# Performance work log

Hardware: AMD Instinct MI355X
Metric: run time of the kernel (lower is better)

The kernel has to match this reference:

```python
import jax, jax.numpy as jnp
import numpy as np

BATCH_SIZE_PER_IM = 512
FG_FRACTION = 0.25
FG_THRESH = 0.5
BG_THRESH_HI = 0.5
BG_THRESH_LO = 0.0
MAX_FG = int(FG_FRACTION * BATCH_SIZE_PER_IM)  # 128


def _rand_boxes(key, shape):
    a = jax.random.uniform(key, shape + (4,), dtype=jnp.float32)
    ymin = jnp.minimum(a[..., 0], a[..., 2])
    ymax = jnp.maximum(a[..., 0], a[..., 2]) + 1e-3
    xmin = jnp.minimum(a[..., 1], a[..., 3])
    xmax = jnp.maximum(a[..., 1], a[..., 3]) + 1e-3
    return jnp.stack([ymin, xmin, ymax, xmax], axis=-1)


def setup_inputs() -> dict:
    key = jax.random.key(0)
    k1, k2, k3, k4 = jax.random.split(key, 4)
    B, N, G = 32, 8192, 128
    boxes = _rand_boxes(k1, (B, N))
    gt_boxes = _rand_boxes(k2, (B, G))
    gt_labels = jax.random.randint(k3, (B, G), 0, 91, dtype=jnp.int32)
    noise = jax.random.uniform(k4, (B, N + G), dtype=jnp.float32)
    return {"boxes": boxes, "gt_boxes": gt_boxes, "gt_labels": gt_labels, "noise": noise}


def _bbox_overlap(boxes, gt_boxes):
    # boxes: [B, M, 4], gt_boxes: [B, G, 4], layout (ymin, xmin, ymax, xmax)
    b_ymin, b_xmin, b_ymax, b_xmax = [boxes[..., i:i + 1] for i in range(4)]  # [B,M,1]
    g_ymin, g_xmin, g_ymax, g_xmax = [gt_boxes[..., i][:, None, :] for i in range(4)]  # [B,1,G]
    i_ymin = jnp.maximum(b_ymin, g_ymin)
    i_xmin = jnp.maximum(b_xmin, g_xmin)
    i_ymax = jnp.minimum(b_ymax, g_ymax)
    i_xmax = jnp.minimum(b_xmax, g_xmax)
    i_area = jnp.maximum(i_ymax - i_ymin, 0.0) * jnp.maximum(i_xmax - i_xmin, 0.0)  # [B,M,G]
    b_area = (b_ymax - b_ymin) * (b_xmax - b_xmin)           # [B,M,1]
    g_area = (g_ymax - g_ymin) * (g_xmax - g_xmin)           # [B,1,G]
    iou = i_area / (b_area + g_area - i_area)
    # padded gt boxes (filled with -1) get IoU = -1
    padding = jnp.logical_and(i_ymin < 0, i_xmin < 0)
    return jnp.where(padding, -1.0, iou)


def reference(boxes, gt_boxes, gt_labels, noise):
    boxes = jax.lax.stop_gradient(boxes)
    all_boxes = jnp.concatenate([boxes, gt_boxes], axis=1)        # [B, M=N+G, 4]
    iou = _bbox_overlap(all_boxes, gt_boxes)                      # [B, M, G]
    max_ov = jnp.max(iou, axis=2)                                 # [B, M]
    p2l = jnp.argmax(iou, axis=2).astype(jnp.int32)               # [B, M]
    box_t = jnp.take_along_axis(gt_boxes, p2l[..., None], axis=1)  # [B, M, 4]
    cls_t = jnp.take_along_axis(gt_labels, p2l, axis=1)           # [B, M]
    pos = max_ov > FG_THRESH
    neg = jnp.logical_and(max_ov >= BG_THRESH_LO, max_ov < BG_THRESH_HI)
    cls_t = jnp.where(neg, 0, cls_t)
    box_t = jnp.where(neg[..., None], 0.0, box_t)
    p2l = jnp.where(neg, 0, p2l)
    # --- balanced fg/bg subsampling (random scores provided in `noise`) ---
    pos_score = jnp.where(pos, noise, -1.0)
    kth = jax.lax.top_k(pos_score, MAX_FG)[0][:, -1:]             # [B,1] threshold
    sel_pos = jnp.logical_and(pos, pos_score >= kth)              # at most MAX_FG fg
    # selected fg get priority band 2+, bg band [0,1), rest -1
    combined = jnp.where(sel_pos, 2.0 + noise, jnp.where(neg, noise, -1.0))
    _, idx = jax.lax.top_k(combined, BATCH_SIZE_PER_IM)           # [B, K]
    rois = jnp.take_along_axis(all_boxes, idx[..., None], axis=1)      # [B, K, 4]
    sample_box_t = jnp.take_along_axis(box_t, idx[..., None], axis=1)  # [B, K, 4]
    sample_cls_t = jnp.take_along_axis(cls_t, idx, axis=1)             # [B, K]
    sample_p2l = jnp.take_along_axis(p2l, idx, axis=1)                 # [B, K]
    return sample_box_t, sample_cls_t, rois, sample_p2l
```

## Files before the change

### kernel.cpp

```cpp
#include <hip/hip_runtime.h>
#include <stdint.h>

#define BATCH 32
#define NBOX 8192
#define NGT 128
#define M (NBOX + NGT)
#define K_OUT 512
#define MAX_FG 128
#define C_CAP 256
#define S_CAP 256
#define U_CAP 1024

__device__ __forceinline__ unsigned int bkt1024(float ns) {
    unsigned int u = (unsigned int)(ns * 16777216.0f) >> 14;
    return u > 1023u ? 1023u : u;
}

__global__ __launch_bounds__(256) void iou_kernel(
    const float* __restrict__ boxes,
    const float* __restrict__ gt_boxes,
    unsigned short* __restrict__ packed)
{
    const int BPB = (M + 255) / 256;
    const int b = blockIdx.x / BPB;
    const int m = (blockIdx.x % BPB) * 256 + threadIdx.x;

    __shared__ float4 sgt[NGT];
    __shared__ float  sgarea[NGT];
    if (threadIdx.x < NGT) {
        float4 g = ((const float4*)gt_boxes)[b * NGT + threadIdx.x];
        sgt[threadIdx.x] = g;
        sgarea[threadIdx.x] = __fmul_rn(__fsub_rn(g.z, g.x), __fsub_rn(g.w, g.y));
    }
    __syncthreads();
    if (m >= M) return;

    float4 bb = (m < NBOX) ? ((const float4*)boxes)[b * NBOX + m]
                           : ((const float4*)gt_boxes)[b * NGT + (m - NBOX)];
    float b_area = __fmul_rn(__fsub_rn(bb.z, bb.x), __fsub_rn(bb.w, bb.y));

    float best = -1e30f;
    int bidx = 0;
    #pragma unroll 4
    for (int g = 0; g < NGT; ++g) {
        float4 gg = sgt[g];
        float iymin = fmaxf(bb.x, gg.x);
        float ixmin = fmaxf(bb.y, gg.y);
        float iymax = fminf(bb.z, gg.z);
        float ixmax = fminf(bb.w, gg.w);
        float ia  = __fmul_rn(fmaxf(__fsub_rn(iymax, iymin), 0.0f),
                              fmaxf(__fsub_rn(ixmax, ixmin), 0.0f));
        float den = __fsub_rn(__fadd_rn(b_area, sgarea[g]), ia);
        float iou = __fdiv_rn(ia, den);
        if (iou > best) { best = iou; bidx = g; }
    }
    bool pos = best > 0.5f;
    bool neg = (best >= 0.0f) && (best < 0.5f);
    packed[b * M + m] = (unsigned short)(bidx | (neg ? 256 : 0) | (pos ? 512 : 0));
}

__global__ __launch_bounds__(1024) void select_kernel(
    const float* __restrict__ boxes,
    const float* __restrict__ gt_boxes,
    const int*   __restrict__ gt_labels,
    const float* __restrict__ noise,
    const unsigned short* __restrict__ packed,
    float* __restrict__ out)
{
    const int b = blockIdx.x;
    const int tid = threadIdx.x;

    __shared__ float sh_ns[M];
    __shared__ unsigned int hist[1024];
    __shared__ unsigned int hist2[1024];
    __shared__ unsigned char posmask[M / 8];
    __shared__ unsigned char negmask[M / 8];
    __shared__ float4 sgt[NGT];
    __shared__ int slab[NGT];
    __shared__ float C[C_CAP];
    __shared__ unsigned short slist[S_CAP];
    __shared__ unsigned int ukey[U_CAP];
    __shared__ unsigned short um[U_CAP];
    __shared__ unsigned int sh_Bp, sh_needp, sh_cc, sh_n1a, sh_B, sh_cnt, sh_kth;

    float* out_bt  = out;
    float* out_cls = out + BATCH * K_OUT * 4;
    float* out_roi = out + BATCH * K_OUT * 5;
    float* out_p2l = out + BATCH * K_OUT * 9;

    hist[tid] = 0;
    hist2[tid] = 0;
    if (tid == 0) { sh_cc = 0; sh_n1a = 0; sh_B = 0; sh_cnt = 0; sh_kth = 0xBF800000u; }
    if (tid < NGT) {
        sgt[tid]  = ((const float4*)gt_boxes)[b * NGT + tid];
        slab[tid] = gt_labels[b * NGT + tid];
    }
    __syncthreads();

    {
        const uint4*  pk4 = (const uint4*)(packed + (size_t)b * M);
        const float4* ns4 = (const float4*)(noise + (size_t)b * M);
        for (int c = tid; c < M / 8; c += 1024) {
            uint4 pv = pk4[c];
            float4 n0 = ns4[2 * c], n1v = ns4[2 * c + 1];
            ((float4*)sh_ns)[2 * c] = n0;
            ((float4*)sh_ns)[2 * c + 1] = n1v;
            unsigned short e[8];
            e[0] = (unsigned short)(pv.x & 0xFFFF); e[1] = (unsigned short)(pv.x >> 16);
            e[2] = (unsigned short)(pv.y & 0xFFFF); e[3] = (unsigned short)(pv.y >> 16);
            e[4] = (unsigned short)(pv.z & 0xFFFF); e[5] = (unsigned short)(pv.z >> 16);
            e[6] = (unsigned short)(pv.w & 0xFFFF); e[7] = (unsigned short)(pv.w >> 16);
            float f[8] = {n0.x, n0.y, n0.z, n0.w, n1v.x, n1v.y, n1v.z, n1v.w};
            unsigned int pb = 0, nb = 0;
            #pragma unroll
            for (int k = 0; k < 8; ++k) {
                if (e[k] & 512) {
                    pb |= (1u << k);
                    atomicAdd(&hist2[bkt1024(f[k])], 1u);
                } else if (e[k] & 256) {
                    nb |= (1u << k);
                    atomicAdd(&hist[bkt1024(f[k])], 1u);
                }
            }
            posmask[c] = (unsigned char)pb;
            negmask[c] = (unsigned char)nb;
        }
    }
    __syncthreads();

    {
        const int wv = tid >> 6, ln = tid & 63;
        if (wv < 2) {
            unsigned int* H = wv ? hist2 : hist;
            unsigned int s[16];
            #pragma unroll
            for (int k = 0; k < 16; ++k) {
                unsigned int v = H[k * 64 + ln];
                #pragma unroll
                for (int off = 1; off < 64; off <<= 1) {
                    unsigned int o = __shfl_down(v, off, 64);
                    if (ln + off < 64) v += o;
                }
                s[k] = v;
            }
            unsigned int after = 0;
            #pragma unroll
            for (int k = 15; k >= 0; --k) {
                unsigned int tot = __shfl(s[k], 0, 64);
                H[k * 64 + ln] = s[k] + after;
                after += tot;
            }
        }
    }
    __syncthreads();
    const unsigned int nneg = hist[0];
    const unsigned int npos = hist2[0];

    if (npos >= MAX_FG) {
        {
            unsigned int S  = hist2[tid];
            unsigned int Sn = (tid < 1023) ? hist2[tid + 1] : 0;
            if (S >= MAX_FG && Sn < MAX_FG) { sh_Bp = tid; sh_needp = MAX_FG - Sn; }
        }
        __syncthreads();
        const unsigned int Bp = sh_Bp, needp = sh_needp;
        for (int c = tid; c < M / 8; c += 1024) {
            unsigned int pb = posmask[c];
            while (pb) {
                int k = __ffs(pb) - 1; pb &= pb - 1;
                float v = sh_ns[c * 8 + k];
                if (bkt1024(v) == Bp) {
                    unsigned int slot = atomicAdd(&sh_cc, 1u);
                    if (slot < C_CAP) C[slot] = v;
                }
            }
        }
        __syncthreads();
        {
            unsigned int cc = min(sh_cc, (unsigned int)C_CAP);
            if (tid < (int)cc) {
                float my = C[tid];
                unsigned int g = 0, e = 0;
                for (unsigned int j = 0; j < cc; ++j) {
                    float v = C[j];
                    g += (v > my) ? 1u : 0u;
                    e += (v == my) ? 1u : 0u;
                }
                if (g < needp && g + e >= needp) sh_kth = __float_as_uint(my);
            }
        }
        __syncthreads();
    }
    const float kthf = __uint_as_float(sh_kth);

    for (int c = tid; c < M / 8; c += 1024) {
        unsigned int pb = posmask[c];
        while (pb) {
            int k = __ffs(pb) - 1; pb &= pb - 1;
            int m = c * 8 + k;
            if (sh_ns[m] >= kthf) {
                unsigned int slot = atomicAdd(&sh_n1a, 1u);
                if (slot < S_CAP) slist[slot] = (unsigned short)m;
            }
        }
    }
    __syncthreads();
    const unsigned int n1 = min(sh_n1a, (unsigned int)S_CAP);
    const unsigned int k2 = K_OUT - n1;
    const bool enough_neg = (nneg >= k2);

    if (enough_neg) {
        unsigned int S  = hist[tid];
        unsigned int Sn = (tid < 1023) ? hist[tid + 1] : 0;
        if (S >= k2 && Sn < k2) sh_B = tid;
    }
    if (tid < (int)n1) {
        int mi = slist[tid];
        float nsi = sh_ns[mi];
        float ci = __fadd_rn(2.0f, nsi);
        unsigned int r = 0;
        for (unsigned int j = 0; j < n1; ++j) {
            int mj = slist[j];
            float cj = __fadd_rn(2.0f, sh_ns[mj]);
            if (cj > ci || (cj == ci && mj < mi)) ++r;
        }
        int pkv = packed[(size_t)b * M + mi];
        int lbl = pkv & 127;
        float4 roi = (mi < NBOX) ? ((const float4*)boxes)[b * NBOX + mi]
                                 : sgt[mi - NBOX];
        ((float4*)out_bt)[b * K_OUT + r] = sgt[lbl];
        out_cls[b * K_OUT + r] = (float)slab[lbl];
        ((float4*)out_roi)[b * K_OUT + r] = roi;
        out_p2l[b * K_OUT + r] = (float)lbl;
    }
    __syncthreads();
    const unsigned int B1 = sh_B;

    for (int c = tid; c < M / 8; c += 1024) {
        unsigned int nb = negmask[c];
        while (nb) {
            int k = __ffs(nb) - 1; nb &= nb - 1;
            int m = c * 8 + k;
            float v = sh_ns[m];
            if (bkt1024(v) >= B1) {
                unsigned int slot = atomicAdd(&sh_cnt, 1u);
                if (slot < U_CAP) {
                    ukey[slot] = __float_as_uint(v);
                    um[slot]   = (unsigned short)m;
                }
            }
        }
    }
    __syncthreads();

    const unsigned int q = min(sh_cnt, (unsigned int)U_CAP);
    for (unsigned int i = tid; i < q; i += 1024) {
        unsigned int ki = ukey[i];
        unsigned short mi = um[i];
        unsigned int r = 0;
        for (unsigned int j = 0; j < q; ++j) {
            unsigned int kj = ukey[j];
            if (kj > ki || (kj == ki && um[j] < mi)) ++r;
        }
        if (r < k2) {
            float4 roi = (mi < NBOX) ? ((const float4*)boxes)[b * NBOX + mi]
                                     : sgt[mi - NBOX];
            unsigned int gr = n1 + r;
            ((float4*)out_bt)[b * K_OUT + gr] = make_float4(0.f, 0.f, 0.f, 0.f);
            out_cls[b * K_OUT + gr] = 0.0f;
            ((float4*)out_roi)[b * K_OUT + gr] = roi;
            out_p2l[b * K_OUT + gr] = 0.0f;
        }
    }

    if (!enough_neg) {
        __syncthreads();
        const unsigned int k3 = k2 - nneg;
        for (int m = tid; m < M; m += 1024) {
            if (((posmask[m >> 3] >> (m & 7)) & 1) && sh_ns[m] < kthf) {
                unsigned int r = 0;
                for (int m2 = 0; m2 < m; ++m2)
                    if (((posmask[m2 >> 3] >> (m2 & 7)) & 1) && sh_ns[m2] < kthf) ++r;
                if (r < k3) {
                    int pkv = packed[(size_t)b * M + m];
                    int lbl = pkv & 127;
                    float4 roi = (m < NBOX) ? ((const float4*)boxes)[b * NBOX + m]
                                            : sgt[m - NBOX];
                    unsigned int gr = n1 + nneg + r;
                    ((float4*)out_bt)[b * K_OUT + gr] = sgt[lbl];
                    out_cls[b * K_OUT + gr] = (float)slab[lbl];
                    ((float4*)out_roi)[b * K_OUT + gr] = roi;
                    out_p2l[b * K_OUT + gr] = (float)lbl;
                }
            }
        }
    }
}

extern "C" void kernel_launch(void* const* d_in, const int* in_sizes, int n_in,
                              void* d_out, int out_size, void* d_ws, size_t ws_size,
                              hipStream_t stream) {
    const float* boxes     = (const float*)d_in[0];
    const float* gt_boxes  = (const float*)d_in[1];
    const int*   gt_labels = (const int*)d_in[2];
    const float* noise     = (const float*)d_in[3];
    unsigned short* packed = (unsigned short*)d_ws;
    float* out = (float*)d_out;

    const int BPB = (M + 255) / 256;
    iou_kernel<<<BATCH * BPB, 256, 0, stream>>>(boxes, gt_boxes, packed);
    select_kernel<<<BATCH, 1024, 0, stream>>>(boxes, gt_boxes, gt_labels, noise,
                                              packed, out);
}
```

Before: 116.0 us.

## Rework IoU staging and select-kernel compaction with register-held noise and wave ballots

The IoU kernel drops its shared-memory GT staging and barrier, reading GT boxes directly from global memory and recomputing their areas each iteration. It also moves to 128-thread blocks sized to divide M exactly. The select kernel keeps each thread's eight noise values and pos/neg masks in registers so later passes skip re-reading shared memory. Negative-candidate compaction switches to wave-level ballot plus one atomic per wave, and the rank loop reads four keys at a time through vector loads over padded arrays. The trade-offs are redundant area arithmetic, uniform global loads in place of LDS reads, and higher register pressure.

```diff
diff --git a/kernel.cpp b/kernel.cpp
--- a/kernel.cpp
+++ b/kernel.cpp
@@ -16,41 +16,49 @@
     return u > 1023u ? 1023u : u;
 }
 
-__global__ __launch_bounds__(256) void iou_kernel(
+template <typename F>
+__device__ __forceinline__ void wave_compact(bool pred, unsigned int* ctr,
+                                             unsigned int cap, F writer) {
+    unsigned long long mb = __ballot(pred);
+    if (!mb) return;
+    const int lane = threadIdx.x & 63;
+    const int leader = __ffsll((unsigned long long)mb) - 1;
+    unsigned int base = 0;
+    if (lane == leader) base = atomicAdd(ctr, (unsigned int)__popcll(mb));
+    base = __shfl(base, leader, 64);
+    if (pred) {
+        unsigned int slot = base + (unsigned int)__popcll(mb & ((1ull << lane) - 1ull));
+        if (slot < cap) writer(slot);
+    }
+}
+
+__global__ __launch_bounds__(128) void iou_kernel(
     const float* __restrict__ boxes,
     const float* __restrict__ gt_boxes,
     unsigned short* __restrict__ packed)
 {
-    const int BPB = (M + 255) / 256;
-    const int b = blockIdx.x / BPB;
-    const int m = (blockIdx.x % BPB) * 256 + threadIdx.x;
-
-    __shared__ float4 sgt[NGT];
-    __shared__ float  sgarea[NGT];
-    if (threadIdx.x < NGT) {
-        float4 g = ((const float4*)gt_boxes)[b * NGT + threadIdx.x];
-        sgt[threadIdx.x] = g;
-        sgarea[threadIdx.x] = __fmul_rn(__fsub_rn(g.z, g.x), __fsub_rn(g.w, g.y));
-    }
-    __syncthreads();
-    if (m >= M) return;
+    const int b = blockIdx.x / 65;
+    const int m = (blockIdx.x % 65) * 128 + threadIdx.x;
+
+    const float4* __restrict__ gt4 = (const float4*)gt_boxes + b * NGT;
 
     float4 bb = (m < NBOX) ? ((const float4*)boxes)[b * NBOX + m]
-                           : ((const float4*)gt_boxes)[b * NGT + (m - NBOX)];
+                           : gt4[m - NBOX];
     float b_area = __fmul_rn(__fsub_rn(bb.z, bb.x), __fsub_rn(bb.w, bb.y));
 
     float best = -1e30f;
     int bidx = 0;
-    #pragma unroll 4
+    #pragma unroll 8
     for (int g = 0; g < NGT; ++g) {
-        float4 gg = sgt[g];
+        float4 gg = gt4[g];
+        float ga = __fmul_rn(__fsub_rn(gg.z, gg.x), __fsub_rn(gg.w, gg.y));
         float iymin = fmaxf(bb.x, gg.x);
         float ixmin = fmaxf(bb.y, gg.y);
         float iymax = fminf(bb.z, gg.z);
         float ixmax = fminf(bb.w, gg.w);
         float ia  = __fmul_rn(fmaxf(__fsub_rn(iymax, iymin), 0.0f),
                               fmaxf(__fsub_rn(ixmax, ixmin), 0.0f));
-        float den = __fsub_rn(__fadd_rn(b_area, sgarea[g]), ia);
+        float den = __fsub_rn(__fadd_rn(b_area, ga), ia);
         float iou = __fdiv_rn(ia, den);
         if (iou > best) { best = iou; bidx = g; }
     }
@@ -79,8 +87,8 @@
     __shared__ int slab[NGT];
     __shared__ float C[C_CAP];
     __shared__ unsigned short slist[S_CAP];
-    __shared__ unsigned int ukey[U_CAP];
-    __shared__ unsigned short um[U_CAP];
+    __shared__ __align__(16) unsigned int   ukey[U_CAP + 4];
+    __shared__ __align__(16) unsigned short um[U_CAP + 4];
     __shared__ unsigned int sh_Bp, sh_needp, sh_cc, sh_n1a, sh_B, sh_cnt, sh_kth;
 
     float* out_bt  = out;
@@ -97,21 +105,23 @@
     }
     __syncthreads();
 
+    float f[8];
+    unsigned int pb = 0, nb = 0;
     {
         const uint4*  pk4 = (const uint4*)(packed + (size_t)b * M);
         const float4* ns4 = (const float4*)(noise + (size_t)b * M);
-        for (int c = tid; c < M / 8; c += 1024) {
-            uint4 pv = pk4[c];
-            float4 n0 = ns4[2 * c], n1v = ns4[2 * c + 1];
-            ((float4*)sh_ns)[2 * c] = n0;
-            ((float4*)sh_ns)[2 * c + 1] = n1v;
+        {
+            uint4 pv = pk4[tid];
+            float4 n0 = ns4[2 * tid], n1v = ns4[2 * tid + 1];
+            ((float4*)sh_ns)[2 * tid] = n0;
+            ((float4*)sh_ns)[2 * tid + 1] = n1v;
+            f[0] = n0.x; f[1] = n0.y; f[2] = n0.z; f[3] = n0.w;
+            f[4] = n1v.x; f[5] = n1v.y; f[6] = n1v.z; f[7] = n1v.w;
             unsigned short e[8];
             e[0] = (unsigned short)(pv.x & 0xFFFF); e[1] = (unsigned short)(pv.x >> 16);
             e[2] = (unsigned short)(pv.y & 0xFFFF); e[3] = (unsigned short)(pv.y >> 16);
             e[4] = (unsigned short)(pv.z & 0xFFFF); e[5] = (unsigned short)(pv.z >> 16);
             e[6] = (unsigned short)(pv.w & 0xFFFF); e[7] = (unsigned short)(pv.w >> 16);
-            float f[8] = {n0.x, n0.y, n0.z, n0.w, n1v.x, n1v.y, n1v.z, n1v.w};
-            unsigned int pb = 0, nb = 0;
             #pragma unroll
             for (int k = 0; k < 8; ++k) {
                 if (e[k] & 512) {
@@ -122,8 +132,34 @@
                     atomicAdd(&hist[bkt1024(f[k])], 1u);
                 }
             }
-            posmask[c] = (unsigned char)pb;
-            negmask[c] = (unsigned char)nb;
+            posmask[tid] = (unsigned char)pb;
+            negmask[tid] = (unsigned char)nb;
+        }
+        if (tid < 16) {
+            int c = 1024 + tid;
+            uint4 pv = pk4[c];
+            float4 n0 = ns4[2 * c], n1v = ns4[2 * c + 1];
+            ((float4*)sh_ns)[2 * c] = n0;
+            ((float4*)sh_ns)[2 * c + 1] = n1v;
+            float ft[8] = {n0.x, n0.y, n0.z, n0.w, n1v.x, n1v.y, n1v.z, n1v.w};
+            unsigned short e[8];
+            e[0] = (unsigned short)(pv.x & 0xFFFF); e[1] = (unsigned short)(pv.x >> 16);
+            e[2] = (unsigned short)(pv.y & 0xFFFF); e[3] = (unsigned short)(pv.y >> 16);
+            e[4] = (unsigned short)(pv.z & 0xFFFF); e[5] = (unsigned short)(pv.z >> 16);
+            e[6] = (unsigned short)(pv.w & 0xFFFF); e[7] = (unsigned short)(pv.w >> 16);
+            unsigned int pb2 = 0, nb2 = 0;
+            #pragma unroll
+            for (int k = 0; k < 8; ++k) {
+                if (e[k] & 512) {
+                    pb2 |= (1u << k);
+                    atomicAdd(&hist2[bkt1024(ft[k])], 1u);
+                } else if (e[k] & 256) {
+                    nb2 |= (1u << k);
+                    atomicAdd(&hist[bkt1024(ft[k])], 1u);
+                }
+            }
+            posmask[c] = (unsigned char)pb2;
+            negmask[c] = (unsigned char)nb2;
         }
     }
     __syncthreads();
@@ -164,14 +200,23 @@
         }
         __syncthreads();
         const unsigned int Bp = sh_Bp, needp = sh_needp;
-        for (int c = tid; c < M / 8; c += 1024) {
-            unsigned int pb = posmask[c];
-            while (pb) {
-                int k = __ffs(pb) - 1; pb &= pb - 1;
-                float v = sh_ns[c * 8 + k];
-                if (bkt1024(v) == Bp) {
-                    unsigned int slot = atomicAdd(&sh_cc, 1u);
-                    if (slot < C_CAP) C[slot] = v;
+        #pragma unroll
+        for (int k = 0; k < 8; ++k) {
+            if (((pb >> k) & 1u) && bkt1024(f[k]) == Bp) {
+                unsigned int slot = atomicAdd(&sh_cc, 1u);
+                if (slot < C_CAP) C[slot] = f[k];
+            }
+        }
+        if (tid < 16) {
+            unsigned int pb2 = posmask[1024 + tid];
+            #pragma unroll
+            for (int k = 0; k < 8; ++k) {
+                if ((pb2 >> k) & 1u) {
+                    float v = sh_ns[(1024 + tid) * 8 + k];
+                    if (bkt1024(v) == Bp) {
+                        unsigned int slot = atomicAdd(&sh_cc, 1u);
+                        if (slot < C_CAP) C[slot] = v;
+                    }
                 }
             }
         }
@@ -193,14 +238,23 @@
     }
     const float kthf = __uint_as_float(sh_kth);
 
-    for (int c = tid; c < M / 8; c += 1024) {
-        unsigned int pb = posmask[c];
-        while (pb) {
-            int k = __ffs(pb) - 1; pb &= pb - 1;
-            int m = c * 8 + k;
-            if (sh_ns[m] >= kthf) {
-                unsigned int slot = atomicAdd(&sh_n1a, 1u);
-                if (slot < S_CAP) slist[slot] = (unsigned short)m;
+    #pragma unroll
+    for (int k = 0; k < 8; ++k) {
+        if (((pb >> k) & 1u) && f[k] >= kthf) {
+            unsigned int slot = atomicAdd(&sh_n1a, 1u);
+            if (slot < S_CAP) slist[slot] = (unsigned short)(tid * 8 + k);
+        }
+    }
+    if (tid < 16) {
+        unsigned int pb2 = posmask[1024 + tid];
+        #pragma unroll
+        for (int k = 0; k < 8; ++k) {
+            if ((pb2 >> k) & 1u) {
+                int m = (1024 + tid) * 8 + k;
+                if (sh_ns[m] >= kthf) {
+                    unsigned int slot = atomicAdd(&sh_n1a, 1u);
+                    if (slot < S_CAP) slist[slot] = (unsigned short)m;
+                }
             }
         }
     }
@@ -236,31 +290,46 @@
     __syncthreads();
     const unsigned int B1 = sh_B;
 
-    for (int c = tid; c < M / 8; c += 1024) {
-        unsigned int nb = negmask[c];
-        while (nb) {
-            int k = __ffs(nb) - 1; nb &= nb - 1;
-            int m = c * 8 + k;
-            float v = sh_ns[m];
-            if (bkt1024(v) >= B1) {
-                unsigned int slot = atomicAdd(&sh_cnt, 1u);
-                if (slot < U_CAP) {
-                    ukey[slot] = __float_as_uint(v);
-                    um[slot]   = (unsigned short)m;
-                }
-            }
+    #pragma unroll
+    for (int k = 0; k < 8; ++k) {
+        float v = f[k];
+        bool p = ((nb >> k) & 1u) && bkt1024(v) >= B1;
+        unsigned short mm = (unsigned short)(tid * 8 + k);
+        wave_compact(p, &sh_cnt, U_CAP, [&](unsigned int s) {
+            ukey[s] = __float_as_uint(v);
+            um[s]   = mm;
+        });
+    }
+    {
+        unsigned int nb2 = (tid < 16) ? (unsigned int)negmask[1024 + tid] : 0u;
+        #pragma unroll
+        for (int k = 0; k < 8; ++k) {
+            bool p = (nb2 >> k) & 1u;
+            float v = p ? sh_ns[(1024 + tid) * 8 + k] : 0.0f;
+            p = p && bkt1024(v) >= B1;
+            unsigned short mm = (unsigned short)((1024 + tid) * 8 + k);
+            wave_compact(p, &sh_cnt, U_CAP, [&](unsigned int s) {
+                ukey[s] = __float_as_uint(v);
+                um[s]   = mm;
+            });
         }
     }
     __syncthreads();
 
     const unsigned int q = min(sh_cnt, (unsigned int)U_CAP);
+    if (tid < 4) { ukey[q + tid] = 0u; um[q + tid] = 0xFFFFu; }
+    __syncthreads();
     for (unsigned int i = tid; i < q; i += 1024) {
         unsigned int ki = ukey[i];
         unsigned short mi = um[i];
         unsigned int r = 0;
-        for (unsigned int j = 0; j < q; ++j) {
-            unsigned int kj = ukey[j];
-            if (kj > ki || (kj == ki && um[j] < mi)) ++r;
+        for (unsigned int j = 0; j < q; j += 4) {
+            uint4 kv = *(const uint4*)&ukey[j];
+            ushort4 mv = *(const ushort4*)&um[j];
+            r += (kv.x > ki || (kv.x == ki && mv.x < mi)) ? 1u : 0u;
+            r += (kv.y > ki || (kv.y == ki && mv.y < mi)) ? 1u : 0u;
+            r += (kv.z > ki || (kv.z == ki && mv.z < mi)) ? 1u : 0u;
+            r += (kv.w > ki || (kv.w == ki && mv.w < mi)) ? 1u : 0u;
         }
         if (r < k2) {
             float4 roi = (mi < NBOX) ? ((const float4*)boxes)[b * NBOX + mi]
@@ -307,8 +376,7 @@
     unsigned short* packed = (unsigned short*)d_ws;
     float* out = (float*)d_out;
 
-    const int BPB = (M + 255) / 256;
-    iou_kernel<<<BATCH * BPB, 256, 0, stream>>>(boxes, gt_boxes, packed);
+    iou_kernel<<<BATCH * 65, 128, 0, stream>>>(boxes, gt_boxes, packed);
     select_kernel<<<BATCH, 1024, 0, stream>>>(boxes, gt_boxes, gt_labels, noise,
                                               packed, out);
 }
```

New measurement: 121.1 us. 1.04x slower.
